# Optimization experiments

Measured on AMD Instinct MI355X. Metric: run time of the kernel, lower is better.

## Reference

```python
import jax, jax.numpy as jnp
import numpy as np

B, J, D, H = 4096, 17, 512, 8
DK = D // H  # 64
NEG = jnp.float32(-9e15)


def _build_adj_mask():
    # Human3.6M 17-joint skeleton (parent indices), symmetric + self-loops,
    # matching SemGCN's adj>0 mask (adj_mx_from_edges adds identity).
    parents = np.array([-1, 0, 1, 2, 0, 4, 5, 0, 7, 8, 9, 8, 11, 12, 8, 14, 15])
    A = np.eye(J, dtype=np.float32)
    for c, p in enumerate(parents):
        if p >= 0:
            A[c, p] = 1.0
            A[p, c] = 1.0
    rows, cols = np.nonzero(A)
    return rows.astype(np.int32), cols.astype(np.int32)


def setup_inputs() -> dict:
    key = jax.random.key(0)
    ks = jax.random.split(key, 16)
    s = 0.02
    rows, cols = _build_adj_mask()
    return {
        "src": jax.random.normal(ks[0], (B, J, D), jnp.float32),
        # per-head Q/K/V Linears, stacked over heads: [H, D, DK]
        "Wq": jax.random.normal(ks[1], (H, D, DK), jnp.float32) * s,
        "bq": jnp.zeros((H, DK), jnp.float32),
        "Wk": jax.random.normal(ks[2], (H, D, DK), jnp.float32) * s,
        "bk": jnp.zeros((H, DK), jnp.float32),
        "Wv": jax.random.normal(ks[3], (H, D, DK), jnp.float32) * s,
        "bv": jnp.zeros((H, DK), jnp.float32),
        # output projection of MultiHeadAttention: [H*DK, D]
        "Wo": jax.random.normal(ks[4], (H * DK, D), jnp.float32) * s,
        "bo": jnp.zeros((D,), jnp.float32),
        "ln1_g": jnp.ones((D,), jnp.float32),
        "ln1_b": jnp.zeros((D,), jnp.float32),
        # SemGraphConv: two weight matrices [2, D, D], edge logits e, bias
        "W_gcn": jax.random.normal(ks[5], (2, D, D), jnp.float32) * s,
        "e_gcn": jax.random.normal(ks[6], (rows.shape[0],), jnp.float32),
        "b_gcn": jnp.zeros((D,), jnp.float32),
        "ln2_g": jnp.ones((D,), jnp.float32),
        "ln2_b": jnp.zeros((D,), jnp.float32),
        "mask_rows": jnp.asarray(rows),
        "mask_cols": jnp.asarray(cols),
    }


def _layernorm(x, g, b, eps=1e-5):
    mu = jnp.mean(x, axis=-1, keepdims=True)
    var = jnp.var(x, axis=-1, keepdims=True)
    return (x - mu) * jax.lax.rsqrt(var + eps) * g + b


def _forward(src, Wq, bq, Wk, bk, Wv, bv, Wo, bo, ln1_g, ln1_b,
             W_gcn, e_gcn, b_gcn, ln2_g, ln2_b, mask_rows, mask_cols):
    # --- multi-head attention (all heads vectorized) ---
    q = jnp.einsum('bjd,hde->bhje', src, Wq) + bq[None, :, None, :]
    k = jnp.einsum('bjd,hde->bhje', src, Wk) + bk[None, :, None, :]
    v = jnp.einsum('bjd,hde->bhje', src, Wv) + bv[None, :, None, :]
    scale = jnp.float32(DK) ** 0.5  # q.size(-1) ** 0.5
    att = jax.nn.softmax(jnp.einsum('bhje,bhke->bhjk', q, k) / scale, axis=-1)
    o = jnp.einsum('bhjk,bhke->bhje', att, v)          # [B,H,J,DK]
    o = o.transpose(0, 2, 1, 3).reshape(B, J, H * DK)  # concat over heads
    attn_out = o @ Wo + bo
    x = _layernorm(src + attn_out, ln1_g, ln1_b)

    # --- SemGraphConv ---
    h0 = x @ W_gcn[0]
    h1 = x @ W_gcn[1]
    logits = jnp.full((J, J), NEG, jnp.float32).at[mask_rows, mask_cols].set(e_gcn)
    A = jax.nn.softmax(logits, axis=1)                 # [J,J]
    I = jnp.eye(J, dtype=jnp.float32)
    gcn = jnp.einsum('jk,bkd->bjd', A * I, h0) + jnp.einsum('jk,bkd->bjd', A * (1.0 - I), h1)
    gcn = gcn + b_gcn
    return _layernorm(x + gcn, ln2_g, ln2_b)


def reference(src, Wq, bq, Wk, bk, Wv, bv, Wo, bo, ln1_g, ln1_b,
              W_gcn, e_gcn, b_gcn, ln2_g, ln2_b, mask_rows, mask_cols):
    return _forward(src, Wq, bq, Wk, bk, Wv, bv, Wo, bo, ln1_g, ln1_b,
                    W_gcn, e_gcn, b_gcn, ln2_g, ln2_b, mask_rows, mask_cols)
```

## Files before the change

kernel.cpp:

```cpp
#include <hip/hip_runtime.h>


typedef __attribute__((ext_vector_type(4))) float floatx4;
typedef __attribute__((ext_vector_type(8))) short short8;

#define AS1 __attribute__((address_space(1)))
#define AS3 __attribute__((address_space(3)))

__device__ __forceinline__ float bf2f(unsigned short u) {
  union { unsigned int i; float f; } x;
  x.i = ((unsigned int)u) << 16;
  return x.f;
}

__device__ __forceinline__ unsigned short f2bf(float f) {
  union { float f; unsigned int i; } x;
  x.f = f;
  unsigned int r = x.i + 0x7fffu + ((x.i >> 16) & 1u);
  return (unsigned short)(r >> 16);
}

__device__ __forceinline__ void unpack8(uint4 u, float* f) {
  unsigned int uu[4] = {u.x, u.y, u.z, u.w};
#pragma unroll
  for (int i = 0; i < 4; ++i) {
    f[2 * i]     = bf2f((unsigned short)(uu[i] & 0xffffu));
    f[2 * i + 1] = bf2f((unsigned short)(uu[i] >> 16));
  }
}

__device__ __forceinline__ uint4 pack8(const float* f) {
  unsigned int uu[4];
#pragma unroll
  for (int i = 0; i < 4; ++i)
    uu[i] = (unsigned int)f2bf(f[2 * i]) | ((unsigned int)f2bf(f[2 * i + 1]) << 16);
  uint4 u; u.x = uu[0]; u.y = uu[1]; u.z = uu[2]; u.w = uu[3];
  return u;
}

__device__ __forceinline__ float wave_sum(float v) {
#pragma unroll
  for (int m = 1; m < 64; m <<= 1) v += __shfl_xor(v, m, 64);
  return v;
}

__device__ __forceinline__ void gload_lds16(const unsigned short* g, AS3 char* l) {
  __builtin_amdgcn_global_load_lds((const AS1 void*)g, (AS3 void*)l, 16, 0, 0);
}

__global__ __launch_bounds__(256) void convert_src(
    const float* __restrict__ in, unsigned short* __restrict__ out) {
  const size_t i = ((size_t)blockIdx.x * 256 + threadIdx.x) * 8;
  const float4 a = *(const float4*)(in + i);
  const float4 b = *(const float4*)(in + i + 4);
  const float f[8] = {a.x, a.y, a.z, a.w, b.x, b.y, b.z, b.w};
  *(uint4*)(out + i) = pack8(f);
}

__global__ __launch_bounds__(256) void gemm_bt(
    const unsigned short* __restrict__ A,
    const unsigned short* __restrict__ BT,
    const float* __restrict__ bias,
    unsigned short* __restrict__ C, int N) {
  __shared__ unsigned short As[3][128 * 32];
  __shared__ unsigned short Bs[3][128 * 32];
  const int t = threadIdx.x;
  const int wave = t >> 6;
  const int lane = t & 63;
  const int wm = wave >> 1, wn = wave & 1;

  const int nTN = N >> 7;
  const int q8 = gridDim.x >> 3;
  const int lin = (blockIdx.x & 7) * q8 + (blockIdx.x >> 3);
  const int tm = lin / nTN;
  const int tn = lin - tm * nTN;
  const long rowBase = (long)tm * 128;
  const long colBase = (long)tn * 128;

  const unsigned short* a0 = A + (size_t)rowBase * 512;
  const unsigned short* b0 = BT + (size_t)colBase * 512;

  floatx4 acc[4][4];
#pragma unroll
  for (int i = 0; i < 4; ++i)
#pragma unroll
    for (int j = 0; j < 4; ++j) acc[i][j] = (floatx4){0.f, 0.f, 0.f, 0.f};

  const int c0 = t, c1 = t + 256;
  const size_t gOff0 =
      (size_t)(c0 >> 2) * 512 + (size_t)((c0 & 3) ^ ((c0 >> 3) & 3)) * 8;
  const size_t gOff1 =
      (size_t)(c1 >> 2) * 512 + (size_t)((c1 & 3) ^ ((c1 >> 3) & 3)) * 8;
  const int ldsByte0 = wave * 1024;
  const int ldsByte1 = 4096 + wave * 1024;

#define STAGE(buf, k0)                                                       \
  do {                                                                       \
    gload_lds16(a0 + gOff0 + (k0), (AS3 char*)&As[(buf)][0] + ldsByte0);     \
    gload_lds16(a0 + gOff1 + (k0), (AS3 char*)&As[(buf)][0] + ldsByte1);     \
    gload_lds16(b0 + gOff0 + (k0), (AS3 char*)&Bs[(buf)][0] + ldsByte0);     \
    gload_lds16(b0 + gOff1 + (k0), (AS3 char*)&Bs[(buf)][0] + ldsByte1);     \
  } while (0)

  const int am = lane & 15;
  const int q = lane >> 4;

  STAGE(0, 0);
  STAGE(1, 32);
  asm volatile("s_waitcnt vmcnt(4)" ::: "memory");
  __builtin_amdgcn_sched_barrier(0);
  __builtin_amdgcn_s_barrier();

#pragma unroll
  for (int kt = 0; kt < 16; ++kt) {
    if (kt + 2 < 16) STAGE((kt + 2) % 3, (kt + 2) * 32);

    const unsigned short* As_ = &As[kt % 3][0];
    const unsigned short* Bs_ = &Bs[kt % 3][0];
    short8 af[4], bf[4];
#pragma unroll
    for (int i = 0; i < 4; ++i) {
      const int row = wm * 64 + i * 16 + am;
      af[i] = *(const short8*)&As_[row * 32 + ((q ^ ((row >> 1) & 3)) << 3)];
    }
#pragma unroll
    for (int j = 0; j < 4; ++j) {
      const int row = wn * 64 + j * 16 + am;
      bf[j] = *(const short8*)&Bs_[row * 32 + ((q ^ ((row >> 1) & 3)) << 3)];
    }
#pragma unroll
    for (int i = 0; i < 4; ++i)
#pragma unroll
      for (int j = 0; j < 4; ++j)
        acc[i][j] = __builtin_amdgcn_mfma_f32_16x16x32_bf16(af[i], bf[j], acc[i][j], 0, 0, 0);

    if (kt == 15) break;
    if (kt < 14) asm volatile("s_waitcnt vmcnt(4)" ::: "memory");
    else         asm volatile("s_waitcnt vmcnt(0)" ::: "memory");
    __builtin_amdgcn_sched_barrier(0);
    __builtin_amdgcn_s_barrier();
  }
#undef STAGE

  const int q4 = (lane >> 4) << 2;
#pragma unroll
  for (int i = 0; i < 4; ++i) {
#pragma unroll
    for (int j = 0; j < 4; ++j) {
      const long col = colBase + wn * 64 + j * 16 + am;
      const float badd = bias ? bias[col] : 0.f;
      const long rowa = rowBase + wm * 64 + i * 16 + q4;
#pragma unroll
      for (int r = 0; r < 4; ++r)
        C[(size_t)(rowa + r) * N + col] = f2bf(acc[i][j][r] + badd);
    }
  }
}

__global__ __launch_bounds__(256) void attn_kernel(
    const unsigned short* __restrict__ qkv, unsigned short* __restrict__ o) {
  const int b = blockIdx.x, h = blockIdx.y;
  __shared__ float q[17][65], k[17][65], v[17][65];
  __shared__ float S[17][17];
  const int t = threadIdx.x;
  const unsigned short* base = qkv + (size_t)b * 17 * 1536 + h * 64;

  for (int idx = t; idx < 3 * 136; idx += 256) {
    const int m = idx / 136, rem = idx - m * 136;
    const int r = rem >> 3, e0 = (rem & 7) << 3;
    uint4 u = *(const uint4*)(base + (size_t)r * 1536 + m * 512 + e0);
    float f[8];
    unpack8(u, f);
    float(*dst)[65] = (m == 0) ? q : (m == 1) ? k : v;
#pragma unroll
    for (int e = 0; e < 8; ++e) dst[r][e0 + e] = f[e];
  }
  __syncthreads();

  for (int idx = t; idx < 289; idx += 256) {
    const int j = idx / 17, kk = idx - j * 17;
    float s = 0.f;
#pragma unroll 8
    for (int e = 0; e < 64; ++e) s += q[j][e] * k[kk][e];
    S[j][kk] = s * 0.125f;
  }
  __syncthreads();

  if (t < 17) {
    float m = -1e30f;
#pragma unroll
    for (int kk = 0; kk < 17; ++kk) m = fmaxf(m, S[t][kk]);
    float tmp[17], sum = 0.f;
#pragma unroll
    for (int kk = 0; kk < 17; ++kk) { tmp[kk] = __expf(S[t][kk] - m); sum += tmp[kk]; }
    const float inv = 1.f / sum;
#pragma unroll
    for (int kk = 0; kk < 17; ++kk) S[t][kk] = tmp[kk] * inv;
  }
  __syncthreads();

  unsigned short* ob = o + (size_t)b * 17 * 512 + h * 64;
  for (int idx = t; idx < 136; idx += 256) {
    const int j = idx >> 3, e0 = (idx & 7) << 3;
    float ov[8] = {0, 0, 0, 0, 0, 0, 0, 0};
#pragma unroll
    for (int kk = 0; kk < 17; ++kk) {
      const float a = S[j][kk];
#pragma unroll
      for (int e = 0; e < 8; ++e) ov[e] += a * v[kk][e0 + e];
    }
    *(uint4*)(ob + (size_t)j * 512 + e0) = pack8(ov);
  }
}

__global__ __launch_bounds__(256) void ln_res_kernel(
    const float* __restrict__ a, const unsigned short* __restrict__ b,
    const float* __restrict__ g, const float* __restrict__ beta,
    unsigned short* __restrict__ out) {
  const long row = (long)blockIdx.x * 4 + (threadIdx.x >> 6);
  const int lane = threadIdx.x & 63;
  const int d0 = lane * 8;

  const float4 a0 = *(const float4*)(a + (size_t)row * 512 + d0);
  const float4 a1 = *(const float4*)(a + (size_t)row * 512 + d0 + 4);
  const float fa[8] = {a0.x, a0.y, a0.z, a0.w, a1.x, a1.y, a1.z, a1.w};
  float fb[8], vals[8];
  unpack8(*(const uint4*)(b + (size_t)row * 512 + d0), fb);
  float s = 0.f, s2 = 0.f;
#pragma unroll
  for (int i = 0; i < 8; ++i) {
    vals[i] = fa[i] + fb[i];
    s += vals[i];
    s2 += vals[i] * vals[i];
  }
  const float mean = wave_sum(s) * (1.f / 512.f);
  const float var = wave_sum(s2) * (1.f / 512.f) - mean * mean;
  const float rs = rsqrtf(var + 1e-5f);

  const float4 g0 = *(const float4*)(g + d0);
  const float4 g1 = *(const float4*)(g + d0 + 4);
  const float4 b0 = *(const float4*)(beta + d0);
  const float4 b1 = *(const float4*)(beta + d0 + 4);
  const float fg[8]  = {g0.x, g0.y, g0.z, g0.w, g1.x, g1.y, g1.z, g1.w};
  const float fbt[8] = {b0.x, b0.y, b0.z, b0.w, b1.x, b1.y, b1.z, b1.w};
  float y[8];
#pragma unroll
  for (int i = 0; i < 8; ++i) y[i] = (vals[i] - mean) * rs * fg[i] + fbt[i];
  *(uint4*)(out + (size_t)row * 512 + d0) = pack8(y);
}

__global__ __launch_bounds__(256) void gcn_ln_kernel(
    const unsigned short* __restrict__ x, const unsigned short* __restrict__ h01,
    const float* __restrict__ Adiag, const int* __restrict__ cnt,
    const int* __restrict__ nbrk, const float* __restrict__ nbrw,
    const float* __restrict__ bgcn,
    const float* __restrict__ g, const float* __restrict__ beta,
    float* __restrict__ out) {
  const long row = (long)blockIdx.x * 4 + (threadIdx.x >> 6);
  const int lane = threadIdx.x & 63;
  const int b = (int)(row / 17);
  const int j = (int)(row - (long)b * 17);
  const int d0 = lane * 8;

  float accv[8];
  {
    const float w = Adiag[j];
    float f[8];
    unpack8(*(const uint4*)(h01 + (size_t)row * 1024 + d0), f);
#pragma unroll
    for (int i = 0; i < 8; ++i) accv[i] = w * f[i];
  }
  const int c = cnt[j];
  for (int nb = 0; nb < c; ++nb) {
    const int kk = nbrk[j * 8 + nb];
    const float w = nbrw[j * 8 + nb];
    float f[8];
    unpack8(*(const uint4*)(h01 + ((size_t)b * 17 + kk) * 1024 + 512 + d0), f);
#pragma unroll
    for (int i = 0; i < 8; ++i) accv[i] += w * f[i];
  }

  float fx[8], vals[8];
  unpack8(*(const uint4*)(x + (size_t)row * 512 + d0), fx);
  const float4 bg0 = *(const float4*)(bgcn + d0);
  const float4 bg1 = *(const float4*)(bgcn + d0 + 4);
  const float fbg[8] = {bg0.x, bg0.y, bg0.z, bg0.w, bg1.x, bg1.y, bg1.z, bg1.w};
  float s = 0.f, s2 = 0.f;
#pragma unroll
  for (int i = 0; i < 8; ++i) {
    vals[i] = fx[i] + accv[i] + fbg[i];
    s += vals[i];
    s2 += vals[i] * vals[i];
  }
  const float mean = wave_sum(s) * (1.f / 512.f);
  const float var = wave_sum(s2) * (1.f / 512.f) - mean * mean;
  const float rs = rsqrtf(var + 1e-5f);

  const float4 g0 = *(const float4*)(g + d0);
  const float4 g1 = *(const float4*)(g + d0 + 4);
  const float4 bb0 = *(const float4*)(beta + d0);
  const float4 bb1 = *(const float4*)(beta + d0 + 4);
  const float fg[8]  = {g0.x, g0.y, g0.z, g0.w, g1.x, g1.y, g1.z, g1.w};
  const float fbt[8] = {bb0.x, bb0.y, bb0.z, bb0.w, bb1.x, bb1.y, bb1.z, bb1.w};
  float4 y0, y1;
  y0.x = (vals[0] - mean) * rs * fg[0] + fbt[0];
  y0.y = (vals[1] - mean) * rs * fg[1] + fbt[1];
  y0.z = (vals[2] - mean) * rs * fg[2] + fbt[2];
  y0.w = (vals[3] - mean) * rs * fg[3] + fbt[3];
  y1.x = (vals[4] - mean) * rs * fg[4] + fbt[4];
  y1.y = (vals[5] - mean) * rs * fg[5] + fbt[5];
  y1.z = (vals[6] - mean) * rs * fg[6] + fbt[6];
  y1.w = (vals[7] - mean) * rs * fg[7] + fbt[7];
  *(float4*)(out + (size_t)row * 512 + d0) = y0;
  *(float4*)(out + (size_t)row * 512 + d0 + 4) = y1;
}

__global__ __launch_bounds__(256) void prep_transpose(
    const float* __restrict__ Wq, const float* __restrict__ Wk,
    const float* __restrict__ Wv, const float* __restrict__ Wo,
    const float* __restrict__ Wg,
    unsigned short* __restrict__ WT1, unsigned short* __restrict__ WT2,
    unsigned short* __restrict__ WT3) {
  const int idx = blockIdx.x * 256 + threadIdx.x;
  if (idx < 786432) {
    const int n = idx >> 9, k = idx & 511;
    const int which = n >> 9, nn = n & 511;
    const int hh = nn >> 6, e = nn & 63;
    const float* W = (which == 0) ? Wq : (which == 1) ? Wk : Wv;
    WT1[idx] = f2bf(W[hh * 32768 + k * 64 + e]);
  } else if (idx < 786432 + 262144) {
    const int i2 = idx - 786432;
    const int n = i2 >> 9, k = i2 & 511;
    WT2[i2] = f2bf(Wo[k * 512 + n]);
  } else {
    const int i3 = idx - 1048576;
    const int n = i3 >> 9, k = i3 & 511;
    const int which = n >> 9, nn = n & 511;
    WT3[i3] = f2bf(Wg[which * 262144 + k * 512 + nn]);
  }
}

__global__ __launch_bounds__(256) void prep_small(
    const float* __restrict__ bq, const float* __restrict__ bk,
    const float* __restrict__ bv, const float* __restrict__ bo,
    const float* __restrict__ e, const int* __restrict__ rows,
    const int* __restrict__ cols, int nnz,
    float* __restrict__ bias1, float* __restrict__ bias2,
    float* __restrict__ Adiag, int* __restrict__ cnt,
    int* __restrict__ nbrk, float* __restrict__ nbrw) {
  const int t = threadIdx.x;
  for (int i = t; i < 1536; i += 256)
    bias1[i] = (i < 512) ? bq[i] : (i < 1024) ? bk[i - 512] : bv[i - 1024];
  for (int i = t; i < 512; i += 256) bias2[i] = bo[i];
  if (t < 17) {
    float m = -1e30f;
    for (int i = 0; i < nnz; ++i)
      if (rows[i] == t) m = fmaxf(m, e[i]);
    float s = 0.f;
    for (int i = 0; i < nnz; ++i)
      if (rows[i] == t) s += __expf(e[i] - m);
    const float inv = 1.f / s;
    int c = 0;
    for (int i = 0; i < nnz; ++i)
      if (rows[i] == t) {
        const float w = __expf(e[i] - m) * inv;
        const int kk = cols[i];
        if (kk == t) Adiag[t] = w;
        else { nbrk[t * 8 + c] = kk; nbrw[t * 8 + c] = w; ++c; }
      }
    cnt[t] = c;
  }
}

extern "C" void kernel_launch(void* const* d_in, const int* in_sizes, int n_in,
                              void* d_out, int out_size, void* d_ws, size_t ws_size,
                              hipStream_t stream) {
  const float* src = (const float*)d_in[0];
  const float* Wq  = (const float*)d_in[1];
  const float* bq  = (const float*)d_in[2];
  const float* Wk  = (const float*)d_in[3];
  const float* bk  = (const float*)d_in[4];
  const float* Wv  = (const float*)d_in[5];
  const float* bv  = (const float*)d_in[6];
  const float* Wo  = (const float*)d_in[7];
  const float* bo  = (const float*)d_in[8];
  const float* ln1g = (const float*)d_in[9];
  const float* ln1b = (const float*)d_in[10];
  const float* Wg  = (const float*)d_in[11];
  const float* eg  = (const float*)d_in[12];
  const float* bg  = (const float*)d_in[13];
  const float* ln2g = (const float*)d_in[14];
  const float* ln2b = (const float*)d_in[15];
  const int* mrows = (const int*)d_in[16];
  const int* mcols = (const int*)d_in[17];
  const int nnz = in_sizes[16];

  float* out = (float*)d_out;
  char* ws = (char*)d_ws;

  unsigned short* WT1 = (unsigned short*)(ws + 0x0000000);
  unsigned short* WT2 = (unsigned short*)(ws + 0x0180000);
  unsigned short* WT3 = (unsigned short*)(ws + 0x0200000);
  float* bias1 = (float*)(ws + 0x0300000);
  float* bias2 = (float*)(ws + 0x0302000);
  float* Adiag = (float*)(ws + 0x0303000);
  int* cnt     = (int*)(ws + 0x0303100);
  int* nbrk    = (int*)(ws + 0x0303200);
  float* nbrw  = (float*)(ws + 0x0303600);
  unsigned short* SRCB = (unsigned short*)(ws + 0x0400000);
  unsigned short* QKV  = (unsigned short*)(ws + 0x4800000);
  unsigned short* O    = (unsigned short*)(ws + 0x0400000);
  unsigned short* ATT  = (unsigned short*)(ws + 0x4800000);
  unsigned short* X    = (unsigned short*)(ws + 0x8C00000);
  unsigned short* H01  = (unsigned short*)(ws + 0x0400000);

  (void)n_in; (void)out_size; (void)ws_size;

  convert_src<<<17408, 256, 0, stream>>>(src, SRCB);
  prep_transpose<<<6144, 256, 0, stream>>>(Wq, Wk, Wv, Wo, Wg, WT1, WT2, WT3);
  prep_small<<<1, 256, 0, stream>>>(bq, bk, bv, bo, eg, mrows, mcols, nnz,
                                    bias1, bias2, Adiag, cnt, nbrk, nbrw);
  gemm_bt<<<6528, 256, 0, stream>>>(SRCB, WT1, bias1, QKV, 1536);
  attn_kernel<<<dim3(4096, 8), 256, 0, stream>>>(QKV, O);
  gemm_bt<<<2176, 256, 0, stream>>>(O, WT2, bias2, ATT, 512);
  ln_res_kernel<<<17408, 256, 0, stream>>>(src, ATT, ln1g, ln1b, X);
  gemm_bt<<<4352, 256, 0, stream>>>(X, WT3, nullptr, H01, 1024);
  gcn_ln_kernel<<<17408, 256, 0, stream>>>(X, H01, Adiag, cnt, nbrk, nbrw, bg,
                                           ln2g, ln2b, out);
}
```

Baseline: 906.4 us.

## Rewrite attention as one wave per (batch, head) using MFMA bf16

Replaces the block-per-(batch,head) scalar attention kernel with one wavefront per (batch,head), four per block. QK^T and PV now run as 16x16x32 bf16 MFMA ops, with the 17th row/column handled by extra tiles and softmax done in registers via cross-lane shuffles. Only V is staged in LDS, per wave, so block-wide __syncthreads are gone. The aim is to cut the large block count and scalar FMA work of the old kernel. The cost is more complex lane-mapping logic, wasted MFMA work on padded tiles, and rounding of probabilities to bf16.

```diff
diff --git a/kernel.cpp b/kernel.cpp
--- a/kernel.cpp
+++ b/kernel.cpp
@@ -159,57 +159,122 @@
 
 __global__ __launch_bounds__(256) void attn_kernel(
     const unsigned short* __restrict__ qkv, unsigned short* __restrict__ o) {
-  const int b = blockIdx.x, h = blockIdx.y;
-  __shared__ float q[17][65], k[17][65], v[17][65];
-  __shared__ float S[17][17];
+  __shared__ unsigned short Vl[4][17][76];
   const int t = threadIdx.x;
+  const int wave = t >> 6, lane = t & 63;
+  const int wid = blockIdx.x * 4 + wave;
+  const int b = wid >> 3, h = wid & 7;
+  const int e = lane & 15, g = lane >> 4;
+
   const unsigned short* base = qkv + (size_t)b * 17 * 1536 + h * 64;
 
-  for (int idx = t; idx < 3 * 136; idx += 256) {
-    const int m = idx / 136, rem = idx - m * 136;
-    const int r = rem >> 3, e0 = (rem & 7) << 3;
-    uint4 u = *(const uint4*)(base + (size_t)r * 1536 + m * 512 + e0);
-    float f[8];
-    unpack8(u, f);
-    float(*dst)[65] = (m == 0) ? q : (m == 1) ? k : v;
-#pragma unroll
-    for (int e = 0; e < 8; ++e) dst[r][e0 + e] = f[e];
-  }
-  __syncthreads();
-
-  for (int idx = t; idx < 289; idx += 256) {
-    const int j = idx / 17, kk = idx - j * 17;
-    float s = 0.f;
-#pragma unroll 8
-    for (int e = 0; e < 64; ++e) s += q[j][e] * k[kk][e];
-    S[j][kk] = s * 0.125f;
-  }
-  __syncthreads();
-
-  if (t < 17) {
-    float m = -1e30f;
-#pragma unroll
-    for (int kk = 0; kk < 17; ++kk) m = fmaxf(m, S[t][kk]);
-    float tmp[17], sum = 0.f;
-#pragma unroll
-    for (int kk = 0; kk < 17; ++kk) { tmp[kk] = __expf(S[t][kk] - m); sum += tmp[kk]; }
+  unsigned short (*V)[76] = Vl[wave];
+  for (int c = lane; c < 136; c += 64) {
+    const int kk = c >> 3, e0 = (c & 7) << 3;
+    const uint4 u = *(const uint4*)(base + (size_t)kk * 1536 + 1024 + e0);
+    *(uint2*)&V[kk][e0]     = make_uint2(u.x, u.y);
+    *(uint2*)&V[kk][e0 + 4] = make_uint2(u.z, u.w);
+  }
+
+  const int ko = g << 3;
+  const unsigned short* qrow  = base + (size_t)e * 1536;
+  const unsigned short* row16 = base + (size_t)16 * 1536;
+  const short8 Q0  = *(const short8*)(qrow + ko);
+  const short8 Q1  = *(const short8*)(qrow + 32 + ko);
+  const short8 K0  = *(const short8*)(qrow + 512 + ko);
+  const short8 K1  = *(const short8*)(qrow + 512 + 32 + ko);
+  const short8 Qb0 = *(const short8*)(row16 + ko);
+  const short8 Qb1 = *(const short8*)(row16 + 32 + ko);
+  const short8 Kb0 = *(const short8*)(row16 + 512 + ko);
+  const short8 Kb1 = *(const short8*)(row16 + 512 + 32 + ko);
+
+  floatx4 sT[2][2];
+#pragma unroll
+  for (int i = 0; i < 2; ++i)
+#pragma unroll
+    for (int j = 0; j < 2; ++j) sT[i][j] = (floatx4){0.f, 0.f, 0.f, 0.f};
+  sT[0][0] = __builtin_amdgcn_mfma_f32_16x16x32_bf16(K0, Q0, sT[0][0], 0, 0, 0);
+  sT[0][0] = __builtin_amdgcn_mfma_f32_16x16x32_bf16(K1, Q1, sT[0][0], 0, 0, 0);
+  sT[0][1] = __builtin_amdgcn_mfma_f32_16x16x32_bf16(K0, Qb0, sT[0][1], 0, 0, 0);
+  sT[0][1] = __builtin_amdgcn_mfma_f32_16x16x32_bf16(K1, Qb1, sT[0][1], 0, 0, 0);
+  sT[1][0] = __builtin_amdgcn_mfma_f32_16x16x32_bf16(Kb0, Q0, sT[1][0], 0, 0, 0);
+  sT[1][0] = __builtin_amdgcn_mfma_f32_16x16x32_bf16(Kb1, Q1, sT[1][0], 0, 0, 0);
+  sT[1][1] = __builtin_amdgcn_mfma_f32_16x16x32_bf16(Kb0, Qb0, sT[1][1], 0, 0, 0);
+  sT[1][1] = __builtin_amdgcn_mfma_f32_16x16x32_bf16(Kb1, Qb1, sT[1][1], 0, 0, 0);
+
+  short8 PA[2];
+#pragma unroll
+  for (int ni = 0; ni < 2; ++ni) {
+    float v[4];
+#pragma unroll
+    for (int r = 0; r < 4; ++r) v[r] = sT[0][ni][r] * 0.125f;
+    const float v16 = sT[1][ni][0] * 0.125f;
+    float m = fmaxf(fmaxf(v[0], v[1]), fmaxf(v[2], v[3]));
+    if (g == 0) m = fmaxf(m, v16);
+    m = fmaxf(m, __shfl_xor(m, 16, 64));
+    m = fmaxf(m, __shfl_xor(m, 32, 64));
+    float p[4], sum = 0.f;
+#pragma unroll
+    for (int r = 0; r < 4; ++r) { p[r] = __expf(v[r] - m); sum += p[r]; }
+    float p16 = (g == 0) ? __expf(v16 - m) : 0.f;
+    sum += p16;
+    sum += __shfl_xor(sum, 16, 64);
+    sum += __shfl_xor(sum, 32, 64);
     const float inv = 1.f / sum;
 #pragma unroll
-    for (int kk = 0; kk < 17; ++kk) S[t][kk] = tmp[kk] * inv;
-  }
-  __syncthreads();
+    for (int r = 0; r < 4; ++r) p[r] *= inv;
+    p16 *= inv;
+
+    const unsigned int lo = (unsigned int)f2bf(p[0]) | ((unsigned int)f2bf(p[1]) << 16);
+    const unsigned int hi = (unsigned int)f2bf(p[2]) | ((unsigned int)f2bf(p[3]) << 16);
+    const unsigned int w16 = (unsigned int)f2bf(p16);
+
+    const int colsrc = ni ? 0 : e;
+    const int s0 = colsrc + ((g & 1) << 5);
+    unsigned int w0 = __shfl(lo, s0, 64);
+    unsigned int w1 = __shfl(hi, s0, 64);
+    unsigned int w2 = __shfl(lo, s0 + 16, 64);
+    unsigned int w3 = __shfl(hi, s0 + 16, 64);
+    const unsigned int a16 = __shfl(w16, colsrc, 64);
+    if (g == 2) { w0 = a16; w1 = 0; w2 = 0; w3 = 0; }
+    if (g == 3) { w0 = 0; w1 = 0; w2 = 0; w3 = 0; }
+    union { unsigned int u[4]; short8 s; } fa;
+    fa.u[0] = w0; fa.u[1] = w1; fa.u[2] = w2; fa.u[3] = w3;
+    PA[ni] = fa.s;
+  }
+
+  floatx4 o0[4], o1[4];
+#pragma unroll
+  for (int tt = 0; tt < 4; ++tt) {
+    o0[tt] = (floatx4){0.f, 0.f, 0.f, 0.f};
+    o1[tt] = (floatx4){0.f, 0.f, 0.f, 0.f};
+  }
+#pragma unroll
+  for (int tt = 0; tt < 4; ++tt) {
+    const int c = tt * 16 + e;
+    union { unsigned int u[4]; short8 s; } fb;
+#pragma unroll
+    for (int i = 0; i < 4; ++i) {
+      int ka = (g << 3) + 2 * i;
+      int kb = ka + 1;
+      if (ka > 16) ka = 16;
+      if (kb > 16) kb = 16;
+      fb.u[i] = (unsigned int)V[ka][c] | ((unsigned int)V[kb][c] << 16);
+    }
+    o0[tt] = __builtin_amdgcn_mfma_f32_16x16x32_bf16(PA[0], fb.s, o0[tt], 0, 0, 0);
+    o1[tt] = __builtin_amdgcn_mfma_f32_16x16x32_bf16(PA[1], fb.s, o1[tt], 0, 0, 0);
+  }
 
   unsigned short* ob = o + (size_t)b * 17 * 512 + h * 64;
-  for (int idx = t; idx < 136; idx += 256) {
-    const int j = idx >> 3, e0 = (idx & 7) << 3;
-    float ov[8] = {0, 0, 0, 0, 0, 0, 0, 0};
-#pragma unroll
-    for (int kk = 0; kk < 17; ++kk) {
-      const float a = S[j][kk];
-#pragma unroll
-      for (int e = 0; e < 8; ++e) ov[e] += a * v[kk][e0 + e];
-    }
-    *(uint4*)(ob + (size_t)j * 512 + e0) = pack8(ov);
+#pragma unroll
+  for (int tt = 0; tt < 4; ++tt)
+#pragma unroll
+    for (int r = 0; r < 4; ++r)
+      ob[(size_t)(4 * g + r) * 512 + tt * 16 + e] = f2bf(o0[tt][r]);
+  if (g == 0) {
+#pragma unroll
+    for (int tt = 0; tt < 4; ++tt)
+      ob[(size_t)16 * 512 + tt * 16 + e] = f2bf(o1[tt][0]);
   }
 }
 
@@ -421,7 +486,7 @@
   prep_small<<<1, 256, 0, stream>>>(bq, bk, bv, bo, eg, mrows, mcols, nnz,
                                     bias1, bias2, Adiag, cnt, nbrk, nbrw);
   gemm_bt<<<6528, 256, 0, stream>>>(SRCB, WT1, bias1, QKV, 1536);
-  attn_kernel<<<dim3(4096, 8), 256, 0, stream>>>(QKV, O);
+  attn_kernel<<<8192, 256, 0, stream>>>(QKV, O);
   gemm_bt<<<2176, 256, 0, stream>>>(O, WT2, bias2, ATT, 512);
   ln_res_kernel<<<17408, 256, 0, stream>>>(src, ATT, ln1g, ln1b, X);
   gemm_bt<<<4352, 256, 0, stream>>>(X, WT3, nullptr, H01, 1024);
```

After: 809.7 us. 1.12x faster.
